# Optimization experiments

Measured on AMD Instinct MI355X. Metric: run time of the kernel, lower is better.

Reference implementation:

```python
import jax, jax.numpy as jnp
import numpy as np

N_NODES = 50000
N_EDGES = 800000
N_REL = 4
D_IN = 128
D_OUT = 128


def setup_inputs() -> dict:
    key = jax.random.key(0)
    ks = jax.random.split(key, 7)
    X = jax.random.normal(ks[0], (N_NODES, D_IN), dtype=jnp.float32)
    rows = jax.random.randint(ks[1], (N_REL, N_EDGES), 0, N_NODES, dtype=jnp.int64)
    cols = jax.random.randint(ks[2], (N_REL, N_EDGES), 0, N_NODES, dtype=jnp.int64)
    vals = jax.random.uniform(ks[3], (N_REL, N_EDGES), dtype=jnp.float32)
    W_rel = jax.random.normal(ks[4], (N_REL, D_IN, D_OUT), dtype=jnp.float32) * (1.0 / np.sqrt(D_IN))
    W_self = jax.random.normal(ks[5], (D_IN, D_OUT), dtype=jnp.float32) * (1.0 / np.sqrt(D_IN))
    bias = jax.random.normal(ks[6], (D_OUT,), dtype=jnp.float32) * 0.01
    return {"X": X, "rows": rows, "cols": cols, "vals": vals,
            "W_rel": W_rel, "W_self": W_self, "bias": bias}


def reference(X, rows, cols, vals, W_rel, W_self, bias):
    """MedGCN multi-relation graph conv: out = X@W_self + sum_r norm(A_r)@X@W_r + b.

    Each A_r given as COO edge list (rows[r], cols[r], vals[r]); duplicate
    indices are summed (matching torch coalesce semantics).
    """
    n = X.shape[0]
    out = X @ W_self + bias
    for r in range(W_rel.shape[0]):
        i, j, v = rows[r], cols[r], vals[r]
        # D^{-1/2} A D^{-1/2}: deg[i] = sum_j A[i, j]
        deg = jax.ops.segment_sum(v, i, num_segments=n)
        inv_sqrt = jnp.clip(deg, 1e-12) ** -0.5
        v_norm = v * inv_sqrt[i] * inv_sqrt[j]
        # spmm: (A_norm @ X)[i] = sum over edges with row i of v_norm * X[j]
        AX = jax.ops.segment_sum(v_norm[:, None] * X[j], i, num_segments=n)
        out = out + AX @ W_rel[r]
    return out
```

## Files before the change

### kernel.cpp

```cpp
#include <hip/hip_runtime.h>
#include <hip/hip_bf16.h>

#define N_NODES 50000
#define N_EDGES 800000
#define N_REL   4
#define D       128
#define NE      (N_REL * N_EDGES)

#define S_SEG   64
#define SEG_E   (NE / S_SEG)
#define G_RANGES 8
#define RPG     (N_NODES / G_RANGES)

#define NCNT    (N_NODES * S_SEG)
#define SCAN_CHUNK 4096
#define NBLK ((NCNT + SCAN_CHUNK - 1) / SCAN_CHUNK)

#define OFF_BST   0
#define OFF_BSUM  12800000
#define OFF_BOFF  12803200
#define OFF_EREC  12806400
#define OFF_Y     38406400
#define OFF_RANK  89606400
#define OFF_INV2  96006400

typedef __attribute__((ext_vector_type(8))) short bf16x8;
typedef __attribute__((ext_vector_type(4))) float f32x4;

__device__ inline unsigned short f2bf(float f) {
    unsigned u = __float_as_uint(f);
    u += 0x7fffu + ((u >> 16) & 1u);
    return (unsigned short)(u >> 16);
}

__global__ __launch_bounds__(256) void k_prep_w(const float* __restrict__ Wself,
                                                const float* __restrict__ Wrel,
                                                unsigned short* __restrict__ Wt) {
    int id = blockIdx.x * 256 + threadIdx.x;
    int seg = id >> 14;
    int rem = id & 16383;
    int n = rem >> 7, k = rem & 127;
    float v = (seg == 0) ? Wself[k * 128 + n] : Wrel[(size_t)(seg - 1) * 16384 + k * 128 + n];
    Wt[id] = f2bf(v);
}

__global__ __launch_bounds__(256) void k_mm(const float* __restrict__ X,
                                            const unsigned short* __restrict__ Wt,
                                            const float* __restrict__ bias,
                                            float* __restrict__ out,
                                            unsigned short* __restrict__ Yb) {
    const int m0 = blockIdx.x * 64;
    const int tid = threadIdx.x;
    const int wave = tid >> 6, lane = tid & 63;
    const int wm = wave >> 1, wn = wave & 1;

    __shared__ unsigned short Xs[64][136];

#pragma unroll
    for (int l = 0; l < 8; l++) {
        int c = tid + l * 256;
        int row = c >> 5, c4 = c & 31;
        int gr = m0 + row;
        float4 v = make_float4(0.f, 0.f, 0.f, 0.f);
        if (gr < N_NODES) v = *(const float4*)(X + (size_t)gr * 128 + c4 * 4);
        ushort4 h;
        h.x = f2bf(v.x); h.y = f2bf(v.y); h.z = f2bf(v.z); h.w = f2bf(v.w);
        *(ushort4*)&Xs[row][c4 * 4] = h;
    }
    __syncthreads();

    const int lr = lane & 15;
    const int kb = (lane >> 4) * 8;
    const int lrow = (lane >> 4) * 4;
    const int lcol = lane & 15;
    const f32x4 zero = {0.f, 0.f, 0.f, 0.f};

    for (int seg = 0; seg < 5; seg++) {
        const unsigned short* Wseg = Wt + (size_t)seg * 16384;
        f32x4 acc[2][4];
#pragma unroll
        for (int i = 0; i < 2; i++)
#pragma unroll
            for (int j = 0; j < 4; j++) acc[i][j] = zero;

#pragma unroll
        for (int k0 = 0; k0 < 128; k0 += 32) {
            bf16x8 a[2], b[4];
#pragma unroll
            for (int i = 0; i < 2; i++)
                a[i] = *(const bf16x8*)&Xs[wm * 32 + i * 16 + lr][k0 + kb];
#pragma unroll
            for (int j = 0; j < 4; j++)
                b[j] = *(const bf16x8*)(Wseg + (size_t)(wn * 64 + j * 16 + lr) * 128 + k0 + kb);
#pragma unroll
            for (int i = 0; i < 2; i++)
#pragma unroll
                for (int j = 0; j < 4; j++)
                    acc[i][j] = __builtin_amdgcn_mfma_f32_16x16x32_bf16(a[i], b[j], acc[i][j], 0, 0, 0);
        }

        if (seg == 0) {
#pragma unroll
            for (int i = 0; i < 2; i++) {
#pragma unroll
                for (int j = 0; j < 4; j++) {
                    int gc = wn * 64 + j * 16 + lcol;
                    float bv = bias[gc];
#pragma unroll
                    for (int v = 0; v < 4; v++) {
                        int gr = m0 + wm * 32 + i * 16 + lrow + v;
                        if (gr < N_NODES)
                            out[(size_t)gr * 128 + gc] = acc[i][j][v] + bv;
                    }
                }
            }
        } else {
            unsigned short* Yseg = Yb + (size_t)(seg - 1) * N_NODES * 128;
#pragma unroll
            for (int i = 0; i < 2; i++) {
#pragma unroll
                for (int j = 0; j < 4; j++) {
                    int gc = wn * 64 + j * 16 + lcol;
#pragma unroll
                    for (int v = 0; v < 4; v++) {
                        int gr = m0 + wm * 32 + i * 16 + lrow + v;
                        if (gr < N_NODES)
                            Yseg[(size_t)gr * 128 + gc] = f2bf(acc[i][j][v]);
                    }
                }
            }
        }
    }
}

__global__ __launch_bounds__(256) void k_count(const int* __restrict__ rows,
                                               int* __restrict__ cntt,
                                               unsigned short* __restrict__ rank) {
    __shared__ int lc[RPG];
    const int seg = blockIdx.x >> 3;
    const int g = blockIdx.x & 7;
    const int rbase = g * RPG;
    for (int i = threadIdx.x; i < RPG; i += 256) lc[i] = 0;
    __syncthreads();
    const int4* r4 = (const int4*)(rows + (size_t)seg * SEG_E);
    const int n4 = SEG_E / 4;
    for (int i = threadIdx.x; i < n4; i += 256) {
        int4 v = r4[i];
        int t = seg * SEG_E + i * 4;
        unsigned int l0 = (unsigned int)(v.x - rbase);
        unsigned int l1 = (unsigned int)(v.y - rbase);
        unsigned int l2 = (unsigned int)(v.z - rbase);
        unsigned int l3 = (unsigned int)(v.w - rbase);
        if (l0 < (unsigned int)RPG) rank[t]     = (unsigned short)atomicAdd(&lc[l0], 1);
        if (l1 < (unsigned int)RPG) rank[t + 1] = (unsigned short)atomicAdd(&lc[l1], 1);
        if (l2 < (unsigned int)RPG) rank[t + 2] = (unsigned short)atomicAdd(&lc[l2], 1);
        if (l3 < (unsigned int)RPG) rank[t + 3] = (unsigned short)atomicAdd(&lc[l3], 1);
    }
    __syncthreads();
    for (int i = threadIdx.x; i < RPG; i += 256)
        cntt[(size_t)seg * N_NODES + rbase + i] = lc[i];
}

__global__ __launch_bounds__(256) void k_tr(const int* __restrict__ cntt,
                                            int* __restrict__ bst) {
    __shared__ int tile[64][65];
    const int r0 = blockIdx.x * 64;
    const int l = threadIdx.x & 63;
    const int q = threadIdx.x >> 6;
#pragma unroll
    for (int p = 0; p < 16; ++p) {
        int seg = q * 16 + p;
        int row = r0 + l;
        tile[seg][l] = (row < N_NODES) ? cntt[(size_t)seg * N_NODES + row] : 0;
    }
    __syncthreads();
#pragma unroll
    for (int p = 0; p < 16; ++p) {
        int rr = q * 16 + p;
        int row = r0 + rr;
        if (row < N_NODES) bst[(size_t)row * S_SEG + l] = tile[l][rr];
    }
}

__global__ __launch_bounds__(256) void k_scanA(int* __restrict__ bst,
                                               int* __restrict__ bsum) {
    __shared__ int s[256];
    int t = threadIdx.x;
    int base = blockIdx.x * SCAN_CHUNK + t * 16;
    int4 v[4];
    int tsum = 0;
#pragma unroll
    for (int q = 0; q < 4; ++q) {
        int idx = base + q * 4;
        if (idx < NCNT) v[q] = *(const int4*)(bst + idx);
        else v[q] = make_int4(0, 0, 0, 0);
        tsum += v[q].x + v[q].y + v[q].z + v[q].w;
    }
    s[t] = tsum;
    __syncthreads();
    for (int off = 1; off < 256; off <<= 1) {
        int x = (t >= off) ? s[t - off] : 0;
        __syncthreads();
        s[t] += x;
        __syncthreads();
    }
    int run = s[t] - tsum;
#pragma unroll
    for (int q = 0; q < 4; ++q) {
        int idx = base + q * 4;
        if (idx < NCNT) {
            int4 o;
            o.x = run; run += v[q].x;
            o.y = run; run += v[q].y;
            o.z = run; run += v[q].z;
            o.w = run; run += v[q].w;
            *(int4*)(bst + idx) = o;
        }
    }
    if (t == 255) bsum[blockIdx.x] = s[255];
}

__global__ __launch_bounds__(256) void k_scanB(const int* __restrict__ bsum,
                                               int* __restrict__ boff) {
    __shared__ int s[256];
    int t = threadIdx.x;
    int b = t * 4;
    int v0 = (b     < NBLK) ? bsum[b]     : 0;
    int v1 = (b + 1 < NBLK) ? bsum[b + 1] : 0;
    int v2 = (b + 2 < NBLK) ? bsum[b + 2] : 0;
    int v3 = (b + 3 < NBLK) ? bsum[b + 3] : 0;
    int tsum = v0 + v1 + v2 + v3;
    s[t] = tsum;
    __syncthreads();
    for (int off = 1; off < 256; off <<= 1) {
        int x = (t >= off) ? s[t - off] : 0;
        __syncthreads();
        s[t] += x;
        __syncthreads();
    }
    int excl = s[t] - tsum;
    if (b     < NBLK) boff[b]     = excl;
    if (b + 1 < NBLK) boff[b + 1] = excl + v0;
    if (b + 2 < NBLK) boff[b + 2] = excl + v0 + v1;
    if (b + 3 < NBLK) boff[b + 3] = excl + v0 + v1 + v2;
}

__global__ __launch_bounds__(256) void k_scanC(int* __restrict__ bst,
                                               const int* __restrict__ boff) {
    int t = threadIdx.x;
    int base = blockIdx.x * SCAN_CHUNK + t * 16;
    int add = boff[blockIdx.x];
#pragma unroll
    for (int q = 0; q < 4; ++q) {
        int idx = base + q * 4;
        if (idx < NCNT) {
            int4 v = *(const int4*)(bst + idx);
            v.x += add; v.y += add; v.z += add; v.w += add;
            *(int4*)(bst + idx) = v;
        }
    }
}

__global__ __launch_bounds__(256) void k_fill(const int* __restrict__ rows,
                                              const int* __restrict__ cols,
                                              const float* __restrict__ vals,
                                              const int* __restrict__ bst,
                                              const unsigned short* __restrict__ rank,
                                              int2* __restrict__ erec) {
    int t = blockIdx.x * 256 + threadIdx.x;
    if (t >= NE) return;
    int seg = t / SEG_E;
    int r = seg >> 4;
    int row = rows[t], col = cols[t];
    int pos = bst[(size_t)row * S_SEG + seg] + (int)rank[t];
    erec[pos] = make_int2(r * N_NODES + col, __float_as_int(vals[t]));
}

__global__ __launch_bounds__(256) void k_deg(const int* __restrict__ bst,
                                             const int2* __restrict__ erec,
                                             float* __restrict__ inv2) {
    int t = blockIdx.x * 256 + threadIdx.x;
    if (t >= N_NODES * 4) return;
    int row = t >> 2, rel = t & 3;
    int s = bst[(size_t)row * S_SEG + rel * 16];
    int e = (rel < 3) ? bst[(size_t)row * S_SEG + rel * 16 + 16]
                      : ((row + 1 < N_NODES) ? bst[(size_t)(row + 1) * S_SEG] : NE);
    float acc = 0.f;
    for (int i = s; i < e; ++i) acc += __int_as_float(erec[i].y);
    inv2[t] = rsqrtf(fmaxf(acc, 1e-12f));
}

__global__ __launch_bounds__(256) void k_gather(const int* __restrict__ bst,
                                                const int2* __restrict__ erec,
                                                const float* __restrict__ inv2,
                                                const unsigned int* __restrict__ Y2,
                                                float* __restrict__ out) {
    const int wid = threadIdx.x >> 6;
    const int lane = threadIdx.x & 63;
    const int row = blockIdx.x * 4 + wid;
    if (row >= N_NODES) return;

    const int start = bst[(size_t)row * S_SEG];
    const int end = (row + 1 < N_NODES) ? bst[(size_t)(row + 1) * S_SEG] : NE;
    const float4 sv = *(const float4*)(inv2 + (size_t)row * 4);

    float ax = 0.f, ay = 0.f;
    for (int base = start; base < end; base += 64) {
        int rem = end - base;
        if (rem > 64) rem = 64;
        int pcL = 0;
        float cfL = 0.f;
        if (lane < rem) {
            int2 rec = erec[base + lane];
            int pc = rec.x;
            int r = (int)((unsigned int)pc / (unsigned int)N_NODES);
            int col = pc - r * N_NODES;
            float selfinv = (r == 0) ? sv.x : (r == 1) ? sv.y : (r == 2) ? sv.z : sv.w;
            cfL = __int_as_float(rec.y) * selfinv * inv2[(size_t)col * 4 + r];
            pcL = pc;
        }
        int c = 0;
        for (; c + 16 <= rem; c += 16) {
            unsigned int y[16];
            float cf[16];
#pragma unroll
            for (int j = 0; j < 16; ++j) {
                int pc = __builtin_amdgcn_readlane(pcL, c + j);
                cf[j] = __int_as_float(__builtin_amdgcn_readlane(__float_as_int(cfL), c + j));
                y[j] = Y2[(size_t)pc * 64 + lane];
            }
#pragma unroll
            for (int j = 0; j < 16; ++j) {
                ax = fmaf(cf[j], __uint_as_float(y[j] << 16), ax);
                ay = fmaf(cf[j], __uint_as_float(y[j] & 0xffff0000u), ay);
            }
        }
        for (; c < rem; ++c) {
            int pc = __builtin_amdgcn_readlane(pcL, c);
            float cf = __int_as_float(__builtin_amdgcn_readlane(__float_as_int(cfL), c));
            unsigned int y = Y2[(size_t)pc * 64 + lane];
            ax = fmaf(cf, __uint_as_float(y << 16), ax);
            ay = fmaf(cf, __uint_as_float(y & 0xffff0000u), ay);
        }
    }
    float2* op = (float2*)(out + (size_t)row * D) + lane;
    float2 o = *op;
    o.x += ax;
    o.y += ay;
    *op = o;
}

extern "C" void kernel_launch(void* const* d_in, const int* in_sizes, int n_in,
                              void* d_out, int out_size, void* d_ws, size_t ws_size,
                              hipStream_t stream) {
    const float* X     = (const float*)d_in[0];
    const int*   rows  = (const int*)d_in[1];
    const int*   cols  = (const int*)d_in[2];
    const float* vals  = (const float*)d_in[3];
    const float* Wrel  = (const float*)d_in[4];
    const float* Wself = (const float*)d_in[5];
    const float* bias  = (const float*)d_in[6];
    float* out = (float*)d_out;

    char* ws = (char*)d_ws;
    int*   bst  = (int*)(ws + OFF_BST);
    int*   bsum = (int*)(ws + OFF_BSUM);
    int*   boff = (int*)(ws + OFF_BOFF);
    int2*  erec = (int2*)(ws + OFF_EREC);
    int*   cntt = (int*)(ws + OFF_EREC);
    unsigned short* Wt = (unsigned short*)(ws + OFF_EREC);
    unsigned short* Yb = (unsigned short*)(ws + OFF_Y);
    unsigned short* rank = (unsigned short*)(ws + OFF_RANK);
    float* inv2 = (float*)(ws + OFF_INV2);

    k_prep_w<<<320, 256, 0, stream>>>(Wself, Wrel, Wt);

    k_mm<<<(N_NODES + 63) / 64, 256, 0, stream>>>(X, Wt, bias, out, Yb);

    k_count<<<S_SEG * G_RANGES, 256, 0, stream>>>(rows, cntt, rank);
    k_tr<<<(N_NODES + 63) / 64, 256, 0, stream>>>(cntt, bst);
    k_scanA<<<NBLK, 256, 0, stream>>>(bst, bsum);
    k_scanB<<<1, 256, 0, stream>>>(bsum, boff);
    k_scanC<<<NBLK, 256, 0, stream>>>(bst, boff);

    k_fill<<<(NE + 255) / 256, 256, 0, stream>>>(rows, cols, vals, bst, rank, erec);
    k_deg<<<(N_NODES * 4 + 255) / 256, 256, 0, stream>>>(bst, erec, inv2);
    k_gather<<<(N_NODES + 3) / 4, 256, 0, stream>>>(bst, erec, inv2,
                                                    (const unsigned int*)Yb, out);
}
```

Baseline: 347.8 us.

## Fuse degree computation into counting pass and pack edges as bf16 coef plus column

Degree sums are now accumulated with shared-memory float atomics in the counting kernel and reduced during the transpose, removing the separate k_deg pass over the sorted edges. The fill kernel precomputes the full normalized coefficient and packs it as bf16 together with a 16-bit column into a single 32-bit record, halving edge record traffic and removing per-edge inverse-sqrt lookups in the gather. The gather loops per relation with a smaller unroll and an occupancy hint. The cost is extra shared atomics in the count kernel and bf16 rounding of the coefficients.

```diff
diff --git a/kernel.cpp b/kernel.cpp
--- a/kernel.cpp
+++ b/kernel.cpp
@@ -19,7 +19,7 @@
 #define OFF_BST   0
 #define OFF_BSUM  12800000
 #define OFF_BOFF  12803200
-#define OFF_EREC  12806400
+#define OFF_SORT  12806400
 #define OFF_Y     38406400
 #define OFF_RANK  89606400
 #define OFF_INV2  96006400
@@ -134,36 +134,46 @@
 }
 
 __global__ __launch_bounds__(256) void k_count(const int* __restrict__ rows,
+                                               const float* __restrict__ vals,
                                                int* __restrict__ cntt,
+                                               float* __restrict__ degt,
                                                unsigned short* __restrict__ rank) {
     __shared__ int lc[RPG];
+    __shared__ float ld[RPG];
     const int seg = blockIdx.x >> 3;
     const int g = blockIdx.x & 7;
     const int rbase = g * RPG;
-    for (int i = threadIdx.x; i < RPG; i += 256) lc[i] = 0;
+    for (int i = threadIdx.x; i < RPG; i += 256) { lc[i] = 0; ld[i] = 0.f; }
     __syncthreads();
     const int4* r4 = (const int4*)(rows + (size_t)seg * SEG_E);
+    const float4* v4 = (const float4*)(vals + (size_t)seg * SEG_E);
     const int n4 = SEG_E / 4;
     for (int i = threadIdx.x; i < n4; i += 256) {
         int4 v = r4[i];
+        float4 w = v4[i];
         int t = seg * SEG_E + i * 4;
         unsigned int l0 = (unsigned int)(v.x - rbase);
         unsigned int l1 = (unsigned int)(v.y - rbase);
         unsigned int l2 = (unsigned int)(v.z - rbase);
         unsigned int l3 = (unsigned int)(v.w - rbase);
-        if (l0 < (unsigned int)RPG) rank[t]     = (unsigned short)atomicAdd(&lc[l0], 1);
-        if (l1 < (unsigned int)RPG) rank[t + 1] = (unsigned short)atomicAdd(&lc[l1], 1);
-        if (l2 < (unsigned int)RPG) rank[t + 2] = (unsigned short)atomicAdd(&lc[l2], 1);
-        if (l3 < (unsigned int)RPG) rank[t + 3] = (unsigned short)atomicAdd(&lc[l3], 1);
-    }
-    __syncthreads();
-    for (int i = threadIdx.x; i < RPG; i += 256)
+        if (l0 < (unsigned int)RPG) { rank[t]     = (unsigned short)atomicAdd(&lc[l0], 1); atomicAdd(&ld[l0], w.x); }
+        if (l1 < (unsigned int)RPG) { rank[t + 1] = (unsigned short)atomicAdd(&lc[l1], 1); atomicAdd(&ld[l1], w.y); }
+        if (l2 < (unsigned int)RPG) { rank[t + 2] = (unsigned short)atomicAdd(&lc[l2], 1); atomicAdd(&ld[l2], w.z); }
+        if (l3 < (unsigned int)RPG) { rank[t + 3] = (unsigned short)atomicAdd(&lc[l3], 1); atomicAdd(&ld[l3], w.w); }
+    }
+    __syncthreads();
+    for (int i = threadIdx.x; i < RPG; i += 256) {
         cntt[(size_t)seg * N_NODES + rbase + i] = lc[i];
+        degt[(size_t)seg * N_NODES + rbase + i] = ld[i];
+    }
 }
 
 __global__ __launch_bounds__(256) void k_tr(const int* __restrict__ cntt,
-                                            int* __restrict__ bst) {
+                                            const float* __restrict__ degt,
+                                            int* __restrict__ bst,
+                                            float* __restrict__ inv2) {
     __shared__ int tile[64][65];
+    __shared__ float dtile[64][65];
     const int r0 = blockIdx.x * 64;
     const int l = threadIdx.x & 63;
     const int q = threadIdx.x >> 6;
@@ -172,6 +182,7 @@
         int seg = q * 16 + p;
         int row = r0 + l;
         tile[seg][l] = (row < N_NODES) ? cntt[(size_t)seg * N_NODES + row] : 0;
+        dtile[seg][l] = (row < N_NODES) ? degt[(size_t)seg * N_NODES + row] : 0.f;
     }
     __syncthreads();
 #pragma unroll
@@ -179,6 +190,14 @@
         int rr = q * 16 + p;
         int row = r0 + rr;
         if (row < N_NODES) bst[(size_t)row * S_SEG + l] = tile[l][rr];
+    }
+    int rowl = threadIdx.x >> 2, rel = threadIdx.x & 3;
+    int row = r0 + rowl;
+    if (row < N_NODES) {
+        float s = 0.f;
+#pragma unroll
+        for (int k = 0; k < 16; ++k) s += dtile[rel * 16 + k][rowl];
+        inv2[(size_t)row * 4 + rel] = rsqrtf(fmaxf(s, 1e-12f));
     }
 }
 
@@ -266,81 +285,62 @@
                                               const float* __restrict__ vals,
                                               const int* __restrict__ bst,
                                               const unsigned short* __restrict__ rank,
-                                              int2* __restrict__ erec) {
+                                              const float* __restrict__ inv2,
+                                              unsigned int* __restrict__ erec) {
     int t = blockIdx.x * 256 + threadIdx.x;
     if (t >= NE) return;
     int seg = t / SEG_E;
     int r = seg >> 4;
     int row = rows[t], col = cols[t];
+    float coef = vals[t] * inv2[(size_t)row * 4 + r] * inv2[(size_t)col * 4 + r];
     int pos = bst[(size_t)row * S_SEG + seg] + (int)rank[t];
-    erec[pos] = make_int2(r * N_NODES + col, __float_as_int(vals[t]));
-}
-
-__global__ __launch_bounds__(256) void k_deg(const int* __restrict__ bst,
-                                             const int2* __restrict__ erec,
-                                             float* __restrict__ inv2) {
-    int t = blockIdx.x * 256 + threadIdx.x;
-    if (t >= N_NODES * 4) return;
-    int row = t >> 2, rel = t & 3;
-    int s = bst[(size_t)row * S_SEG + rel * 16];
-    int e = (rel < 3) ? bst[(size_t)row * S_SEG + rel * 16 + 16]
-                      : ((row + 1 < N_NODES) ? bst[(size_t)(row + 1) * S_SEG] : NE);
-    float acc = 0.f;
-    for (int i = s; i < e; ++i) acc += __int_as_float(erec[i].y);
-    inv2[t] = rsqrtf(fmaxf(acc, 1e-12f));
-}
-
-__global__ __launch_bounds__(256) void k_gather(const int* __restrict__ bst,
-                                                const int2* __restrict__ erec,
-                                                const float* __restrict__ inv2,
-                                                const unsigned int* __restrict__ Y2,
-                                                float* __restrict__ out) {
+    erec[pos] = ((unsigned int)f2bf(coef) << 16) | (unsigned int)col;
+}
+
+__global__ __launch_bounds__(256, 8) void k_gather(const int* __restrict__ bst,
+                                                   const unsigned int* __restrict__ erec,
+                                                   const unsigned int* __restrict__ Y2,
+                                                   float* __restrict__ out) {
     const int wid = threadIdx.x >> 6;
     const int lane = threadIdx.x & 63;
     const int row = blockIdx.x * 4 + wid;
     if (row >= N_NODES) return;
 
-    const int start = bst[(size_t)row * S_SEG];
-    const int end = (row + 1 < N_NODES) ? bst[(size_t)(row + 1) * S_SEG] : NE;
-    const float4 sv = *(const float4*)(inv2 + (size_t)row * 4);
+    const int bend = (row + 1 < N_NODES) ? bst[(size_t)(row + 1) * S_SEG] : NE;
 
     float ax = 0.f, ay = 0.f;
-    for (int base = start; base < end; base += 64) {
-        int rem = end - base;
-        if (rem > 64) rem = 64;
-        int pcL = 0;
-        float cfL = 0.f;
-        if (lane < rem) {
-            int2 rec = erec[base + lane];
-            int pc = rec.x;
-            int r = (int)((unsigned int)pc / (unsigned int)N_NODES);
-            int col = pc - r * N_NODES;
-            float selfinv = (r == 0) ? sv.x : (r == 1) ? sv.y : (r == 2) ? sv.z : sv.w;
-            cfL = __int_as_float(rec.y) * selfinv * inv2[(size_t)col * 4 + r];
-            pcL = pc;
-        }
-        int c = 0;
-        for (; c + 16 <= rem; c += 16) {
-            unsigned int y[16];
-            float cf[16];
-#pragma unroll
-            for (int j = 0; j < 16; ++j) {
-                int pc = __builtin_amdgcn_readlane(pcL, c + j);
-                cf[j] = __int_as_float(__builtin_amdgcn_readlane(__float_as_int(cfL), c + j));
-                y[j] = Y2[(size_t)pc * 64 + lane];
+#pragma unroll
+    for (int rel = 0; rel < 4; ++rel) {
+        const unsigned int* Yr = Y2 + (size_t)rel * N_NODES * 64;
+        const int s = bst[(size_t)row * S_SEG + rel * 16];
+        const int e = (rel < 3) ? bst[(size_t)row * S_SEG + rel * 16 + 16] : bend;
+        for (int base = s; base < e; base += 64) {
+            int rem = e - base;
+            if (rem > 64) rem = 64;
+            unsigned int recL = (lane < rem) ? erec[base + lane] : 0u;
+            int c = 0;
+            for (; c + 8 <= rem; c += 8) {
+                unsigned int y[8];
+                float cf[8];
+#pragma unroll
+                for (int j = 0; j < 8; ++j) {
+                    unsigned int u = (unsigned int)__builtin_amdgcn_readlane((int)recL, c + j);
+                    cf[j] = __uint_as_float(u & 0xffff0000u);
+                    y[j] = Yr[(size_t)(u & 0xffffu) * 64 + lane];
+                }
+#pragma unroll
+                for (int j = 0; j < 8; ++j) {
+                    ax = fmaf(cf[j], __uint_as_float(y[j] << 16), ax);
+                    ay = fmaf(cf[j], __uint_as_float(y[j] & 0xffff0000u), ay);
+                }
             }
-#pragma unroll
-            for (int j = 0; j < 16; ++j) {
-                ax = fmaf(cf[j], __uint_as_float(y[j] << 16), ax);
-                ay = fmaf(cf[j], __uint_as_float(y[j] & 0xffff0000u), ay);
+            for (; c < rem; ++c) {
+                unsigned int u = (unsigned int)__builtin_amdgcn_readlane((int)recL, c);
+                float cf = __uint_as_float(u & 0xffff0000u);
+                unsigned int y = Yr[(size_t)(u & 0xffffu) * 64 + lane];
+                ax = fmaf(cf, __uint_as_float(y << 16), ax);
+                ay = fmaf(cf, __uint_as_float(y & 0xffff0000u), ay);
             }
-        }
-        for (; c < rem; ++c) {
-            int pc = __builtin_amdgcn_readlane(pcL, c);
-            float cf = __int_as_float(__builtin_amdgcn_readlane(__float_as_int(cfL), c));
-            unsigned int y = Y2[(size_t)pc * 64 + lane];
-            ax = fmaf(cf, __uint_as_float(y << 16), ax);
-            ay = fmaf(cf, __uint_as_float(y & 0xffff0000u), ay);
         }
     }
     float2* op = (float2*)(out + (size_t)row * D) + lane;
@@ -366,9 +366,10 @@
     int*   bst  = (int*)(ws + OFF_BST);
     int*   bsum = (int*)(ws + OFF_BSUM);
     int*   boff = (int*)(ws + OFF_BOFF);
-    int2*  erec = (int2*)(ws + OFF_EREC);
-    int*   cntt = (int*)(ws + OFF_EREC);
-    unsigned short* Wt = (unsigned short*)(ws + OFF_EREC);
+    unsigned short* Wt = (unsigned short*)(ws + OFF_SORT);
+    int*   cntt = (int*)(ws + OFF_SORT);
+    float* degt = (float*)(ws + OFF_SORT + 12800000);
+    unsigned int* erec = (unsigned int*)(ws + OFF_SORT);
     unsigned short* Yb = (unsigned short*)(ws + OFF_Y);
     unsigned short* rank = (unsigned short*)(ws + OFF_RANK);
     float* inv2 = (float*)(ws + OFF_INV2);
@@ -377,14 +378,13 @@
 
     k_mm<<<(N_NODES + 63) / 64, 256, 0, stream>>>(X, Wt, bias, out, Yb);
 
-    k_count<<<S_SEG * G_RANGES, 256, 0, stream>>>(rows, cntt, rank);
-    k_tr<<<(N_NODES + 63) / 64, 256, 0, stream>>>(cntt, bst);
+    k_count<<<S_SEG * G_RANGES, 256, 0, stream>>>(rows, vals, cntt, degt, rank);
+    k_tr<<<(N_NODES + 63) / 64, 256, 0, stream>>>(cntt, degt, bst, inv2);
     k_scanA<<<NBLK, 256, 0, stream>>>(bst, bsum);
     k_scanB<<<1, 256, 0, stream>>>(bsum, boff);
     k_scanC<<<NBLK, 256, 0, stream>>>(bst, boff);
 
-    k_fill<<<(NE + 255) / 256, 256, 0, stream>>>(rows, cols, vals, bst, rank, erec);
-    k_deg<<<(N_NODES * 4 + 255) / 256, 256, 0, stream>>>(bst, erec, inv2);
-    k_gather<<<(N_NODES + 3) / 4, 256, 0, stream>>>(bst, erec, inv2,
+    k_fill<<<(NE + 255) / 256, 256, 0, stream>>>(rows, cols, vals, bst, rank, inv2, erec);
+    k_gather<<<(N_NODES + 3) / 4, 256, 0, stream>>>(bst, erec,
                                                     (const unsigned int*)Yb, out);
 }
```

Result: no change. 352.2 us (+1.3%).
